# Performance work log

Measured on AMD Instinct MI355X. Metric: run time of the kernel, lower is better.

The kernel has to match this reference:

```python
import jax, jax.numpy as jnp
import numpy as np

N, E, T = 20000, 320000, 64
INP, EMB, OUT = 128, 16, 3
HEADS, MSIZE, MDIM, KDIM, VDIM = 4, 1024, 128, 64, 64


def setup_inputs() -> dict:
    key = jax.random.key(0)
    ks = iter(jax.random.split(key, 64))

    def nrm(shape, s=0.05):
        return jax.random.normal(next(ks), shape, dtype=jnp.float32) * s

    return dict(
        x=jax.random.normal(next(ks), (N, INP), dtype=jnp.float32),
        edge_index=jax.random.randint(next(ks), (2, E), 0, N),
        index=5,
        inp_types=jax.random.randint(next(ks), (T,), 0, 4),
        log_return=jax.random.normal(next(ks), (T,), dtype=jnp.float32),
        # SAGEConv 1 (SoftmaxAggregation temp t1, lin_l/lin_r, bias=False)
        t1=jnp.ones((1, INP), jnp.float32),
        W1l=nrm((INP, 512)), W1r=nrm((INP, 512)),
        ln1g_w=jnp.ones((512,), jnp.float32), ln1g_b=jnp.zeros((512,), jnp.float32),
        # SAGEConv 2
        t2=jnp.ones((1, 512), jnp.float32),
        W2l=nrm((512, 256)), W2r=nrm((512, 256)),
        ln2g_w=jnp.ones((256,), jnp.float32), ln2g_b=jnp.zeros((256,), jnp.float32),
        # MemPooling(256,128,heads=4,num_clusters=1)
        mp_k=nrm((HEADS, 1, 256), 1.0),
        mp_conv=nrm((HEADS,), 0.5),            # Conv2d(heads,1,1,bias=False)
        mp_lin=nrm((256, 128)),                # Linear(in,out,bias=False)
        fxg_w=nrm((128, 256)), fxg_b=jnp.zeros((256,), jnp.float32),
        # PolicyNet head
        emb=nrm((4, EMB), 1.0),
        fk_w=nrm((256, KDIM)), fk_b=jnp.zeros((KDIM,), jnp.float32),
        fv_w=nrm((256, VDIM)), fv_b=jnp.zeros((VDIM,), jnp.float32),
        # MultiHeadMemory
        mem=nrm((HEADS, MSIZE, MDIM), 1.0),
        mfk_w=nrm((MDIM, KDIM)), mfk_b=jnp.zeros((KDIM,), jnp.float32),
        mfv_w=nrm((MDIM, VDIM)), mfv_b=jnp.zeros((VDIM,), jnp.float32),
        mfx_w=nrm((VDIM * HEADS, VDIM)), mfx_b=jnp.zeros((VDIM,), jnp.float32),
        f1_w=nrm((INP + EMB + 2 * VDIM + 1, 512)),
        n1_w=jnp.ones((512,), jnp.float32), n1_b=jnp.zeros((512,), jnp.float32),
        f2_w=nrm((512, 256)),
        n2_w=jnp.ones((256,), jnp.float32), n2_b=jnp.zeros((256,), jnp.float32),
        f3_w=nrm((256, OUT)), f3_b=jnp.zeros((OUT,), jnp.float32),
    )


def _forward(x, t1, W1l, W1r, ln1g_w, ln1g_b, t2, W2l, W2r, ln2g_w, ln2g_b,
             mp_k, mp_conv, mp_lin, fxg_w, fxg_b, emb, fk_w, fk_b, fv_w, fv_b,
             mem, mfk_w, mfk_b, mfv_w, mfv_b, mfx_w, mfx_b,
             f1_w, n1_w, n1_b, f2_w, n2_w, n2_b, f3_w, f3_b,
             log_return, edge_index, inp_types, index):
    n = x.shape[0]
    src, dst = edge_index[0], edge_index[1]

    def sage(h, t, Wl, Wr):
        hj = h[src]                                    # [E, C] gather
        gate = hj * t                                  # learned softmax temperature
        m = jax.ops.segment_max(gate, dst, num_segments=n)
        e = jnp.exp(gate - m[dst])                     # segment-stable softmax
        s = jax.ops.segment_sum(e, dst, num_segments=n)
        agg = jax.ops.segment_sum(hj * (e / s[dst]), dst, num_segments=n)
        return agg @ Wl + h @ Wr                       # SAGEConv, bias=False

    def graph_ln(h, w, b, eps=1e-5):                   # PyG LayerNorm, mode='graph'
        hc = h - jnp.mean(h)
        return hc / jnp.sqrt(jnp.mean(hc * hc) + eps) * w + b

    h = jax.nn.relu(graph_ln(sage(x, t1, W1l, W1r), ln1g_w, ln1g_b))
    h = jax.nn.relu(graph_ln(sage(h, t2, W2l, W2r), ln2g_w, ln2g_b))

    # MemPooling (single graph => B=1), tau=1: student-t kernel over sq. distances
    H, K, C = mp_k.shape
    kk = mp_k.reshape(H * K, C)
    d2 = jnp.maximum(jnp.sum(kk * kk, 1)[:, None] - 2.0 * (kk @ h.T)
                     + jnp.sum(h * h, 1)[None, :], 0.0)        # [H*K, N]
    dist = 1.0 / (1.0 + d2)
    dist = dist.reshape(H, K, n).transpose(0, 2, 1)[None]      # [1, H, N, K]
    S = dist / jnp.sum(dist, -1, keepdims=True)
    S = jax.nn.softmax(jnp.einsum('h,bhnk->bnk', mp_conv, S), axis=-1)  # [1, N, K]
    zp = jnp.einsum('bnk,nc->bkc', S, h)[:, 0, :]              # squeeze(1), K==1
    z = (zp @ mp_lin) @ fxg_w + fxg_b                          # [1, 256]

    q = jax.nn.softmax(z @ fk_w + fk_b, axis=-1)               # [1, key_dim]
    v = z @ fv_w + fv_b                                        # [1, val_dim]

    # MultiHeadMemory
    km = jax.nn.softmax(mem @ mfk_w + mfk_b, axis=-1)          # [H, M, key]
    vm = mem @ mfv_w + mfv_b                                   # [H, M, val]
    w = jax.nn.softmax(jnp.einsum('bk,hnk->bhn', q, km), axis=-1)
    mv = jnp.einsum('bhn,hnv->bhv', w, vm).reshape(q.shape[0], -1)
    m_out = mv @ mfx_w + mfx_b                                 # [1, val]

    zz = jnp.concatenate([v, m_out], axis=-1)                  # [1, 2*val]
    t_len = inp_types.shape[0]
    xi = jnp.broadcast_to(x[index][None, :], (t_len, x.shape[1]))
    zb = jnp.broadcast_to(zz, (t_len, zz.shape[1]))
    feat = jnp.concatenate([xi, emb[inp_types], log_return.reshape(-1, 1), zb], axis=-1)

    def ln(h2, w2, b2, eps=1e-5):                              # nn.LayerNorm (last dim)
        mu = jnp.mean(h2, -1, keepdims=True)
        hc = h2 - mu
        return hc / jnp.sqrt(jnp.mean(hc * hc, -1, keepdims=True) + eps) * w2 + b2

    h1 = jax.nn.relu(ln(feat @ f1_w, n1_w, n1_b))              # dropout = identity (eval)
    h2 = jax.nn.relu(ln(h1 @ f2_w, n2_w, n2_b))
    return jax.nn.softmax(h2 @ f3_w + f3_b, axis=-1)           # [T, out_dim]


def reference(x, edge_index, index, inp_types, log_return, t1, W1l, W1r, ln1g_w, ln1g_b,
              t2, W2l, W2r, ln2g_w, ln2g_b, mp_k, mp_conv, mp_lin, fxg_w, fxg_b, emb,
              fk_w, fk_b, fv_w, fv_b, mem, mfk_w, mfk_b, mfv_w, mfv_b, mfx_w, mfx_b,
              f1_w, n1_w, n1_b, f2_w, n2_w, n2_b, f3_w, f3_b):
    return _forward(x, t1, W1l, W1r, ln1g_w, ln1g_b, t2, W2l, W2r, ln2g_w, ln2g_b,
                    mp_k, mp_conv, mp_lin, fxg_w, fxg_b, emb, fk_w, fk_b, fv_w, fv_b,
                    mem, mfk_w, mfk_b, mfv_w, mfv_b, mfx_w, mfx_b,
                    f1_w, n1_w, n1_b, f2_w, n2_w, n2_b, f3_w, f3_b,
                    log_return, edge_index, inp_types, index)
```

## Files before the change

kernel.cpp:

```cpp
#include <hip/hip_runtime.h>

typedef __attribute__((ext_vector_type(8))) short bf16x8;
typedef __attribute__((ext_vector_type(8))) unsigned short ushort8_t;
typedef __attribute__((ext_vector_type(4))) float f32x4;

__device__ __forceinline__ unsigned short f2bf(float f) {
    unsigned int x = __float_as_uint(f);
    unsigned int r = x + 0x7fffu + ((x >> 16) & 1u);
    return (unsigned short)(r >> 16);
}
__device__ __forceinline__ float bf2f(unsigned short u) {
    return __uint_as_float(((unsigned int)u) << 16);
}
__device__ __forceinline__ float fexp2(float x) { return __builtin_amdgcn_exp2f(x); }

#define LOG2E 1.44269504089f

__global__ __launch_bounds__(256) void prep_kernel(
    const int* __restrict__ dst, int E, int* __restrict__ counts,
    const float* __restrict__ x, unsigned short* __restrict__ xb, size_t nx4,
    const float* __restrict__ W1l, const float* __restrict__ W1r, unsigned short* __restrict__ Bt1,
    const float* __restrict__ W2l, const float* __restrict__ W2r, unsigned short* __restrict__ Bt2) {
    int i = blockIdx.x * 256 + threadIdx.x;
    int total = gridDim.x * 256;
    if (i < E) atomicAdd(&counts[dst[i]], 1);
    for (size_t j = i; j < nx4; j += total) {
        float4 v = *(const float4*)(x + j * 4);
        ushort4 o;
        o.x = f2bf(v.x); o.y = f2bf(v.y); o.z = f2bf(v.z); o.w = f2bf(v.w);
        *(ushort4*)(xb + j * 4) = o;
    }
    if (i < 512 * 256) {
        int nn = i >> 8, k = i & 255;
        float v = (k < 128) ? W1l[(size_t)k * 512 + nn] : W1r[(size_t)(k - 128) * 512 + nn];
        Bt1[i] = f2bf(v);
    }
    if (i < 256 * 1024) {
        int nn = i >> 10, k = i & 1023;
        float v = (k < 512) ? W2l[(size_t)k * 256 + nn] : W2r[(size_t)(k - 512) * 256 + nn];
        Bt2[i] = f2bf(v);
    }
}

template <int CHUNK>
__global__ __launch_bounds__(1024) void scan_kernel(int* __restrict__ cnt,
                                                    int* __restrict__ off, int n) {
    __shared__ int s[1024];
    int tid = threadIdx.x;
    int base = tid * CHUNK;
    int loc[CHUNK];
    int sum = 0;
#pragma unroll
    for (int i = 0; i < CHUNK; ++i) {
        int idx = base + i;
        int v = 0;
        if (idx < n) { v = cnt[idx]; cnt[idx] = 0; }
        sum += v;
        loc[i] = sum;
    }
    s[tid] = sum;
    __syncthreads();
    for (int d = 1; d < 1024; d <<= 1) {
        int t = (tid >= d) ? s[tid - d] : 0;
        __syncthreads();
        s[tid] += t;
        __syncthreads();
    }
    int prev = (tid > 0) ? s[tid - 1] : 0;
    if (tid == 0) off[0] = 0;
#pragma unroll
    for (int i = 0; i < CHUNK; ++i) {
        int idx = base + i;
        if (idx < n) off[idx + 1] = prev + loc[i];
    }
}

__global__ void fill_kernel(const int* __restrict__ src, const int* __restrict__ dst, int E,
                            const int* __restrict__ off, int* __restrict__ cursor,
                            int* __restrict__ srcs) {
    int i = blockIdx.x * 256 + threadIdx.x;
    if (i < E) {
        int d = dst[i];
        int p = atomicAdd(&cursor[d], 1);
        srcs[off[d] + p] = src[i];
    }
}

__global__ __launch_bounds__(256) void agg512s(const unsigned short* __restrict__ h,
                                               const float* __restrict__ t,
                                               const int* __restrict__ off,
                                               const int* __restrict__ srcs,
                                               unsigned short* __restrict__ agg, int n) {
    int wid = threadIdx.x >> 6, lane = threadIdx.x & 63;
    int node = blockIdx.x * 4 + wid;
    if (node >= n) return;
    int beg = off[node], end = off[node + 1];
    int col = blockIdx.y * 256 + lane * 4;
    float tc0 = t[col] * LOG2E, tc1 = t[col + 1] * LOG2E;
    float tc2 = t[col + 2] * LOG2E, tc3 = t[col + 3] * LOG2E;
    float sE0 = 0.f, sE1 = 0.f, sE2 = 0.f, sE3 = 0.f;
    float sW0 = 0.f, sW1 = 0.f, sW2 = 0.f, sW3 = 0.f;
#define P4(u)                                                        \
    {                                                                \
        float v0 = bf2f(u.x), v1 = bf2f(u.y);                        \
        float v2 = bf2f(u.z), v3 = bf2f(u.w);                        \
        float w0_ = fexp2(v0 * tc0), w1_ = fexp2(v1 * tc1);          \
        float w2_ = fexp2(v2 * tc2), w3_ = fexp2(v3 * tc3);          \
        sE0 += w0_; sW0 += v0 * w0_; sE1 += w1_; sW1 += v1 * w1_;    \
        sE2 += w2_; sW2 += v2 * w2_; sE3 += w3_; sW3 += v3 * w3_;    \
    }
    int e = beg;
    for (; e + 4 <= end; e += 4) {
        ushort4 u0 = *(const ushort4*)(h + (size_t)srcs[e] * 512 + col);
        ushort4 u1 = *(const ushort4*)(h + (size_t)srcs[e + 1] * 512 + col);
        ushort4 u2 = *(const ushort4*)(h + (size_t)srcs[e + 2] * 512 + col);
        ushort4 u3 = *(const ushort4*)(h + (size_t)srcs[e + 3] * 512 + col);
        P4(u0) P4(u1) P4(u2) P4(u3)
    }
    for (; e < end; ++e) {
        ushort4 u0 = *(const ushort4*)(h + (size_t)srcs[e] * 512 + col);
        P4(u0)
    }
#undef P4
    ushort4 o;
    o.x = f2bf((end > beg) ? (sW0 / sE0) : 0.f);
    o.y = f2bf((end > beg) ? (sW1 / sE1) : 0.f);
    o.z = f2bf((end > beg) ? (sW2 / sE2) : 0.f);
    o.w = f2bf((end > beg) ? (sW3 / sE3) : 0.f);
    *(ushort4*)(agg + (size_t)node * 512 + col) = o;
}

__global__ __launch_bounds__(256) void agg128(const unsigned short* __restrict__ h,
                                              const float* __restrict__ t,
                                              const int* __restrict__ off,
                                              const int* __restrict__ srcs,
                                              unsigned short* __restrict__ agg, int n) {
    int wid = threadIdx.x >> 6, lane = threadIdx.x & 63;
    int node = blockIdx.x * 4 + wid;
    if (node >= n) return;
    int beg = off[node], end = off[node + 1];
    int col = lane * 2;
    float t0 = t[col] * LOG2E, t1 = t[col + 1] * LOG2E;
    float e0 = 0.f, e1 = 0.f, w0 = 0.f, w1 = 0.f;
#define P2(u)                                          \
    {                                                  \
        float a = bf2f(u.x), b = bf2f(u.y);            \
        float xa = fexp2(a * t0), xb = fexp2(b * t1);  \
        e0 += xa; e1 += xb; w0 += a * xa; w1 += b * xb; \
    }
    int e = beg;
    for (; e + 4 <= end; e += 4) {
        ushort2 u0 = *(const ushort2*)(h + (size_t)srcs[e] * 128 + col);
        ushort2 u1 = *(const ushort2*)(h + (size_t)srcs[e + 1] * 128 + col);
        ushort2 u2 = *(const ushort2*)(h + (size_t)srcs[e + 2] * 128 + col);
        ushort2 u3 = *(const ushort2*)(h + (size_t)srcs[e + 3] * 128 + col);
        P2(u0) P2(u1) P2(u2) P2(u3)
    }
    for (; e < end; ++e) {
        ushort2 u0 = *(const ushort2*)(h + (size_t)srcs[e] * 128 + col);
        P2(u0)
    }
#undef P2
    ushort2 o;
    o.x = f2bf((end > beg) ? (w0 / e0) : 0.f);
    o.y = f2bf((end > beg) ? (w1 / e1) : 0.f);
    *(ushort2*)(agg + (size_t)node * 128 + col) = o;
}

__global__ __launch_bounds__(256) void gemm_dual_mfma3(
    const unsigned short* __restrict__ A1, const unsigned short* __restrict__ A2,
    const unsigned short* __restrict__ Bt,
    unsigned short* __restrict__ Cb, double* __restrict__ part,
    int M, int N, int K1, int K2) {
    const int Kc = K1 + K2;
    __shared__ unsigned short As[64 * 40];
    __shared__ unsigned short Bs[256 * 40];
    __shared__ double rs[256], rs2[256];
    int tid = threadIdx.x;
    int lane = tid & 63, w = tid >> 6;
    int m0 = blockIdx.y * 64, n0 = blockIdx.x * 256;
    f32x4 acc[4][4] = {};
    int kg = lane >> 4, lr = lane & 15;

    for (int k0 = 0; k0 < Kc; k0 += 32) {
        const unsigned short* Asrc;
        int kk, Ksrc;
        if (k0 < K1) { Asrc = A1; kk = k0; Ksrc = K1; }
        else         { Asrc = A2; kk = k0 - K1; Ksrc = K2; }
        {
            int r = tid >> 2, ch = tid & 3;
            int gr = m0 + r;
            ushort8_t v = {0, 0, 0, 0, 0, 0, 0, 0};
            if (gr < M) v = *(const ushort8_t*)(Asrc + (size_t)gr * Ksrc + kk + ch * 8);
            *(ushort8_t*)&As[r * 40 + ch * 8] = v;
        }
#pragma unroll
        for (int it = 0; it < 4; ++it) {
            int idx = tid + it * 256;
            int r = idx >> 2, ch = idx & 3;
            const unsigned short* srcp = Bt + (size_t)(n0 + r) * Kc + k0 + ch * 8;
            *(ushort8_t*)&Bs[r * 40 + ch * 8] = *(const ushort8_t*)srcp;
        }
        __syncthreads();
        bf16x8 a[4], b[4];
#pragma unroll
        for (int i = 0; i < 4; ++i)
            a[i] = *(bf16x8*)&As[(i * 16 + lr) * 40 + kg * 8];
#pragma unroll
        for (int j = 0; j < 4; ++j)
            b[j] = *(bf16x8*)&Bs[(w * 64 + j * 16 + lr) * 40 + kg * 8];
#pragma unroll
        for (int i = 0; i < 4; ++i)
#pragma unroll
            for (int j = 0; j < 4; ++j)
                acc[i][j] = __builtin_amdgcn_mfma_f32_16x16x32_bf16(a[i], b[j], acc[i][j], 0, 0, 0);
        __syncthreads();
    }
    double s = 0, s2 = 0;
#pragma unroll
    for (int i = 0; i < 4; ++i) {
        int rbase = m0 + i * 16 + kg * 4;
#pragma unroll
        for (int j = 0; j < 4; ++j) {
            int col = n0 + w * 64 + j * 16 + lr;
#pragma unroll
            for (int reg = 0; reg < 4; ++reg) {
                int row = rbase + reg;
                if (row < M) {
                    float v = acc[i][j][reg];
                    Cb[(size_t)row * N + col] = f2bf(v);
                    s += v;
                    s2 += (double)v * v;
                }
            }
        }
    }
    rs[tid] = s;
    rs2[tid] = s2;
    __syncthreads();
    for (int d = 128; d; d >>= 1) {
        if (tid < d) { rs[tid] += rs[tid + d]; rs2[tid] += rs2[tid + d]; }
        __syncthreads();
    }
    if (tid == 0) {
        int bid = blockIdx.y * gridDim.x + blockIdx.x;
        part[bid * 2] = rs[0];
        part[bid * 2 + 1] = rs2[0];
    }
}

template <int C>
__global__ __launch_bounds__(256) void ln_relu_ip(unsigned short* __restrict__ z,
                                                  const float* __restrict__ w,
                                                  const float* __restrict__ b,
                                                  const double* __restrict__ part, int nb,
                                                  float invn, size_t n) {
    __shared__ float st[2];
    if (threadIdx.x < 64) {
        double s = 0, s2 = 0;
        for (int i = threadIdx.x; i < nb; i += 64) { s += part[2 * i]; s2 += part[2 * i + 1]; }
        for (int d = 32; d; d >>= 1) { s += __shfl_down(s, d); s2 += __shfl_down(s2, d); }
        if (threadIdx.x == 0) {
            float mu = (float)(s * invn);
            float var = (float)(s2 * invn) - mu * mu;
            st[0] = mu;
            st[1] = rsqrtf(var + 1e-5f);
        }
    }
    __syncthreads();
    float mu = st[0], inv = st[1];
    size_t stride = (size_t)gridDim.x * 256 * 4;
    for (size_t i = ((size_t)blockIdx.x * 256 + threadIdx.x) * 4; i < n; i += stride) {
        ushort4 v = *(const ushort4*)(z + i);
        int c = (int)(i & (C - 1));
        ushort4 o;
        o.x = f2bf(fmaxf((bf2f(v.x) - mu) * inv * w[c] + b[c], 0.f));
        o.y = f2bf(fmaxf((bf2f(v.y) - mu) * inv * w[c + 1] + b[c + 1], 0.f));
        o.z = f2bf(fmaxf((bf2f(v.z) - mu) * inv * w[c + 2] + b[c + 2], 0.f));
        o.w = f2bf(fmaxf((bf2f(v.w) - mu) * inv * w[c + 3] + b[c + 3], 0.f));
        *(ushort4*)(z + i) = o;
    }
}

__global__ __launch_bounds__(256) void ln_colsum(const unsigned short* __restrict__ z2,
                                                 const float* __restrict__ w,
                                                 const float* __restrict__ b,
                                                 const double* __restrict__ part, int nb,
                                                 float invn, int n,
                                                 float* __restrict__ cspartT) {
    __shared__ float red[8 * 256];
    __shared__ float st[2];
    int tid = threadIdx.x;
    if (tid < 64) {
        double s = 0, s2 = 0;
        for (int i = tid; i < nb; i += 64) { s += part[2 * i]; s2 += part[2 * i + 1]; }
        for (int d = 32; d; d >>= 1) { s += __shfl_down(s, d); s2 += __shfl_down(s2, d); }
        if (tid == 0) {
            float mu = (float)(s * invn);
            float var = (float)(s2 * invn) - mu * mu;
            st[0] = mu;
            st[1] = rsqrtf(var + 1e-5f);
        }
    }
    __syncthreads();
    float mu = st[0], inv = st[1];
    int cg = tid & 31;
    int rl = tid >> 5;
    int c8 = cg * 8;
    float lw[8], lb[8];
#pragma unroll
    for (int i = 0; i < 8; ++i) { lw[i] = w[c8 + i] * inv; lb[i] = b[c8 + i] - mu * inv * w[c8 + i]; }
    int rows_per = (n + gridDim.x - 1) / gridDim.x;
    int r0 = blockIdx.x * rows_per;
    int r1 = min(n, r0 + rows_per);
    float acc[8] = {};
    for (int r = r0 + rl; r < r1; r += 8) {
        ushort8_t u = *(const ushort8_t*)(z2 + (size_t)r * 256 + c8);
#pragma unroll
        for (int i = 0; i < 8; ++i) acc[i] += fmaxf(bf2f(u[i]) * lw[i] + lb[i], 0.f);
    }
#pragma unroll
    for (int i = 0; i < 8; ++i) red[rl * 256 + c8 + i] = acc[i];
    __syncthreads();
    float s = 0;
#pragma unroll
    for (int r = 0; r < 8; ++r) s += red[r * 256 + tid];
    cspartT[tid * 64 + blockIdx.x] = s;
}

__global__ __launch_bounds__(256) void zqv_kernel(const float* __restrict__ cspartT,
                                                  const float* __restrict__ mp_lin,
                                                  const float* __restrict__ fxg_w,
                                                  const float* __restrict__ fxg_b,
                                                  const float* __restrict__ fk_w,
                                                  const float* __restrict__ fk_b,
                                                  const float* __restrict__ fv_w,
                                                  const float* __restrict__ fv_b,
                                                  float* __restrict__ qv) {
    __shared__ float zp_s[256], u_s[128], z_s[256], ql_s[64];
    __shared__ float part_s[1024];
    int tid = threadIdx.x;
    {
        float s = 0;
        const float* p = cspartT + tid * 64;
#pragma unroll
        for (int i = 0; i < 16; ++i) {
            float4 v = *(const float4*)(p + i * 4);
            s += v.x + v.y + v.z + v.w;
        }
        zp_s[tid] = s;
    }
    __syncthreads();
    {
        int og = tid & 31, kc = tid >> 5;
        int j4 = og * 4;
        f32x4 a = {0.f, 0.f, 0.f, 0.f};
        for (int ci = 0; ci < 32; ++ci) {
            int c = kc * 32 + ci;
            float4 w = *(const float4*)(mp_lin + (size_t)c * 128 + j4);
            float zc = zp_s[c];
            a[0] += zc * w.x; a[1] += zc * w.y; a[2] += zc * w.z; a[3] += zc * w.w;
        }
#pragma unroll
        for (int i = 0; i < 4; ++i) part_s[kc * 128 + j4 + i] = a[i];
    }
    __syncthreads();
    if (tid < 128) {
        float s = 0;
#pragma unroll
        for (int kc = 0; kc < 8; ++kc) s += part_s[kc * 128 + tid];
        u_s[tid] = s;
    }
    __syncthreads();
    {
        int og = tid & 63, kc = tid >> 6;
        int j4 = og * 4;
        f32x4 a = {0.f, 0.f, 0.f, 0.f};
        for (int ci = 0; ci < 32; ++ci) {
            int c = kc * 32 + ci;
            float4 w = *(const float4*)(fxg_w + (size_t)c * 256 + j4);
            float uc = u_s[c];
            a[0] += uc * w.x; a[1] += uc * w.y; a[2] += uc * w.z; a[3] += uc * w.w;
        }
#pragma unroll
        for (int i = 0; i < 4; ++i) part_s[kc * 256 + j4 + i] = a[i];
    }
    __syncthreads();
    {
        float s = fxg_b[tid];
#pragma unroll
        for (int kc = 0; kc < 4; ++kc) s += part_s[kc * 256 + tid];
        z_s[tid] = s;
    }
    __syncthreads();
    {
        int og = tid & 15, kc = tid >> 4;
        int j4 = og * 4;
        f32x4 a = {0.f, 0.f, 0.f, 0.f};
        for (int ci = 0; ci < 16; ++ci) {
            int c = kc * 16 + ci;
            float4 w = *(const float4*)(fk_w + (size_t)c * 64 + j4);
            float zc = z_s[c];
            a[0] += zc * w.x; a[1] += zc * w.y; a[2] += zc * w.z; a[3] += zc * w.w;
        }
#pragma unroll
        for (int i = 0; i < 4; ++i) part_s[kc * 64 + j4 + i] = a[i];
    }
    __syncthreads();
    if (tid < 64) {
        float s = fk_b[tid];
#pragma unroll
        for (int kc = 0; kc < 16; ++kc) s += part_s[kc * 64 + tid];
        ql_s[tid] = s;
    }
    __syncthreads();
    {
        int og = tid & 15, kc = tid >> 4;
        int j4 = og * 4;
        f32x4 a = {0.f, 0.f, 0.f, 0.f};
        for (int ci = 0; ci < 16; ++ci) {
            int c = kc * 16 + ci;
            float4 w = *(const float4*)(fv_w + (size_t)c * 64 + j4);
            float zc = z_s[c];
            a[0] += zc * w.x; a[1] += zc * w.y; a[2] += zc * w.z; a[3] += zc * w.w;
        }
#pragma unroll
        for (int i = 0; i < 4; ++i) part_s[kc * 64 + j4 + i] = a[i];
    }
    __syncthreads();
    if (tid < 64) {
        float mx = ql_s[tid];
        for (int d = 32; d; d >>= 1) mx = fmaxf(mx, __shfl_xor(mx, d));
        float e = __expf(ql_s[tid] - mx);
        float s = e;
        for (int d = 32; d; d >>= 1) s += __shfl_xor(s, d);
        qv[tid] = e / s;
        float vv = fv_b[tid];
#pragma unroll
        for (int kc = 0; kc < 16; ++kc) vv += part_s[kc * 64 + tid];
        qv[64 + tid] = vv;
    }
}

__global__ __launch_bounds__(256) void mem_kv_logit(const float* __restrict__ mem,
                                                    const float* __restrict__ mfk_w,
                                                    const float* __restrict__ mfk_b,
                                                    const float* __restrict__ mfv_w,
                                                    const float* __restrict__ mfv_b,
                                                    const float* __restrict__ qv,
                                                    float* __restrict__ logits,
                                                    float* __restrict__ vm) {
    __shared__ float rows[4][128];
    __shared__ float qs[64];
    int tid = threadIdx.x;
    int r0 = blockIdx.x * 4;
    if (tid < 64) qs[tid] = qv[tid];
    for (int i = tid; i < 512; i += 256) rows[i >> 7][i & 127] = mem[(size_t)r0 * 128 + i];
    __syncthreads();
    int lr = tid >> 6;
    int lane = tid & 63;
    const float* row = rows[lr];
    float kl = mfk_b[lane], vl = mfv_b[lane];
#pragma unroll 8
    for (int c = 0; c < 128; ++c) {
        float rv = row[c];
        kl += rv * mfk_w[c * 64 + lane];
        vl += rv * mfv_w[c * 64 + lane];
    }
    float mx = kl;
    for (int d = 32; d; d >>= 1) mx = fmaxf(mx, __shfl_xor(mx, d));
    float e = __expf(kl - mx);
    float s = e;
    for (int d = 32; d; d >>= 1) s += __shfl_xor(s, d);
    float kval = e / s;
    float wl = kval * qs[lane];
    for (int d = 32; d; d >>= 1) wl += __shfl_xor(wl, d);
    size_t gr = (size_t)(r0 + lr);
    if (lane == 0) logits[gr] = wl;
    vm[gr * 64 + lane] = vl;
}

__global__ __launch_bounds__(256) void attend_part(const float* __restrict__ logits,
                                                   const float* __restrict__ vm,
                                                   float* __restrict__ part) {
    int b = blockIdx.x;
    int h = b >> 4;
    int s0 = (b & 15) * 64;
    int tid = threadIdx.x;
    __shared__ float els[64];
    __shared__ float pr[4][64];
    __shared__ float lmax_s, lsum_s;
    if (tid < 64) {
        float lg = logits[h * 1024 + s0 + tid];
        float m = lg;
        for (int d = 32; d; d >>= 1) m = fmaxf(m, __shfl_xor(m, d));
        float e = __expf(lg - m);
        els[tid] = e;
        float s = e;
        for (int d = 32; d; d >>= 1) s += __shfl_xor(s, d);
        if (tid == 0) { lmax_s = m; lsum_s = s; }
    }
    __syncthreads();
    int dd = tid & 63, g = tid >> 6;
    float acc = 0;
    for (int s = g; s < 64; s += 4)
        acc += els[s] * vm[((size_t)h * 1024 + s0 + s) * 64 + dd];
    pr[g][dd] = acc;
    __syncthreads();
    if (tid < 64) {
        float pv = pr[0][tid] + pr[1][tid] + pr[2][tid] + pr[3][tid];
        part[b * 66 + 2 + tid] = pv;
        if (tid == 0) { part[b * 66] = lmax_s; part[b * 66 + 1] = lsum_s; }
    }
}

__device__ __forceinline__ float block_sum_256(float v, float* red) {
    int tid = threadIdx.x;
    red[tid] = v;
    __syncthreads();
    for (int d = 128; d; d >>= 1) { if (tid < d) red[tid] += red[tid + d]; __syncthreads(); }
    float r = red[0];
    __syncthreads();
    return r;
}

__global__ __launch_bounds__(256) void head_kernel(
    const float* __restrict__ x, const int* __restrict__ index_p,
    const int* __restrict__ inp_types, const float* __restrict__ log_return,
    const float* __restrict__ emb, const float* __restrict__ qv,
    const float* __restrict__ apart, const float* __restrict__ mfx_w,
    const float* __restrict__ mfx_b, const float* __restrict__ f1_w,
    const float* __restrict__ n1_w, const float* __restrict__ n1_b,
    const float* __restrict__ f2_w, const float* __restrict__ n2_w,
    const float* __restrict__ n2_b, const float* __restrict__ f3_w,
    const float* __restrict__ f3_b, float* __restrict__ out) {
    __shared__ float feat[273];
    __shared__ float h1[512];
    __shared__ float h2[256];
    __shared__ float red[256];
    __shared__ float l3[3];
    __shared__ float mv_s[256];
    __shared__ float mpart[1024];
    __shared__ float m_out_s[64];
    int r = blockIdx.x, tid = threadIdx.x;
    int idx = index_p[0];
    {
        int h = tid >> 6, dd = tid & 63;
        float gmax = -1e30f;
#pragma unroll
        for (int p = 0; p < 16; ++p) gmax = fmaxf(gmax, apart[(h * 16 + p) * 66]);
        float total = 0.f, acc = 0.f;
#pragma unroll
        for (int p = 0; p < 16; ++p) {
            float sc = __expf(apart[(h * 16 + p) * 66] - gmax);
            total += apart[(h * 16 + p) * 66 + 1] * sc;
            acc += apart[(h * 16 + p) * 66 + 2 + dd] * sc;
        }
        mv_s[h * 64 + dd] = acc / total;
    }
    __syncthreads();
    {
        int og = tid & 15, kc = tid >> 4;
        int j4 = og * 4;
        f32x4 a = {0.f, 0.f, 0.f, 0.f};
        for (int ci = 0; ci < 16; ++ci) {
            int c = kc * 16 + ci;
            float4 w = *(const float4*)(mfx_w + (size_t)c * 64 + j4);
            float mc = mv_s[c];
            a[0] += mc * w.x; a[1] += mc * w.y; a[2] += mc * w.z; a[3] += mc * w.w;
        }
#pragma unroll
        for (int i = 0; i < 4; ++i) mpart[kc * 64 + j4 + i] = a[i];
    }
    __syncthreads();
    if (tid < 64) {
        float s = mfx_b[tid];
#pragma unroll
        for (int kc = 0; kc < 16; ++kc) s += mpart[kc * 64 + tid];
        m_out_s[tid] = s;
    }
    __syncthreads();
    for (int i = tid; i < 273; i += 256) {
        float val;
        if (i < 128) val = x[(size_t)idx * 128 + i];
        else if (i < 144) val = emb[inp_types[r] * 16 + (i - 128)];
        else if (i == 144) val = log_return[r];
        else if (i < 209) val = qv[64 + (i - 145)];
        else val = m_out_s[i - 209];
        feat[i] = val;
    }
    __syncthreads();
    float a0 = 0, a1 = 0;
    for (int c = 0; c < 273; ++c) {
        float f = feat[c];
        a0 += f * f1_w[c * 512 + tid];
        a1 += f * f1_w[c * 512 + tid + 256];
    }
    float mu = block_sum_256(a0 + a1, red) / 512.f;
    float c0 = a0 - mu, c1 = a1 - mu;
    float var = block_sum_256(c0 * c0 + c1 * c1, red) / 512.f;
    float inv = rsqrtf(var + 1e-5f);
    h1[tid] = fmaxf(c0 * inv * n1_w[tid] + n1_b[tid], 0.f);
    h1[tid + 256] = fmaxf(c1 * inv * n1_w[tid + 256] + n1_b[tid + 256], 0.f);
    __syncthreads();
    float b0 = 0;
    for (int c = 0; c < 512; ++c) b0 += h1[c] * f2_w[c * 256 + tid];
    float mu2 = block_sum_256(b0, red) / 256.f;
    float cc = b0 - mu2;
    float var2 = block_sum_256(cc * cc, red) / 256.f;
    float inv2 = rsqrtf(var2 + 1e-5f);
    h2[tid] = fmaxf(cc * inv2 * n2_w[tid] + n2_b[tid], 0.f);
    __syncthreads();
    if (tid < 3) {
        float a = f3_b[tid];
        for (int c = 0; c < 256; ++c) a += h2[c] * f3_w[c * 3 + tid];
        l3[tid] = a;
    }
    __syncthreads();
    if (tid < 3) {
        float mx = fmaxf(l3[0], fmaxf(l3[1], l3[2]));
        float s = __expf(l3[0] - mx) + __expf(l3[1] - mx) + __expf(l3[2] - mx);
        out[r * 3 + tid] = __expf(l3[tid] - mx) / s;
    }
}

extern "C" void kernel_launch(void* const* d_in, const int* in_sizes, int n_in,
                              void* d_out, int out_size, void* d_ws, size_t ws_size,
                              hipStream_t stream) {
    const float* x = (const float*)d_in[0];
    const int* ei = (const int*)d_in[1];
    const int* index_p = (const int*)d_in[2];
    const int* inp_types = (const int*)d_in[3];
    const float* log_return = (const float*)d_in[4];
    const float* t1 = (const float*)d_in[5];
    const float* W1l = (const float*)d_in[6];
    const float* W1r = (const float*)d_in[7];
    const float* ln1g_w = (const float*)d_in[8];
    const float* ln1g_b = (const float*)d_in[9];
    const float* t2 = (const float*)d_in[10];
    const float* W2l = (const float*)d_in[11];
    const float* W2r = (const float*)d_in[12];
    const float* ln2g_w = (const float*)d_in[13];
    const float* ln2g_b = (const float*)d_in[14];
    const float* mp_lin = (const float*)d_in[17];
    const float* fxg_w = (const float*)d_in[18];
    const float* fxg_b = (const float*)d_in[19];
    const float* emb = (const float*)d_in[20];
    const float* fk_w = (const float*)d_in[21];
    const float* fk_b = (const float*)d_in[22];
    const float* fv_w = (const float*)d_in[23];
    const float* fv_b = (const float*)d_in[24];
    const float* mem = (const float*)d_in[25];
    const float* mfk_w = (const float*)d_in[26];
    const float* mfk_b = (const float*)d_in[27];
    const float* mfv_w = (const float*)d_in[28];
    const float* mfv_b = (const float*)d_in[29];
    const float* mfx_w = (const float*)d_in[30];
    const float* mfx_b = (const float*)d_in[31];
    const float* f1_w = (const float*)d_in[32];
    const float* n1_w = (const float*)d_in[33];
    const float* n1_b = (const float*)d_in[34];
    const float* f2_w = (const float*)d_in[35];
    const float* n2_w = (const float*)d_in[36];
    const float* n2_b = (const float*)d_in[37];
    const float* f3_w = (const float*)d_in[38];
    const float* f3_b = (const float*)d_in[39];
    float* out = (float*)d_out;

    int n = in_sizes[0] / 128;
    int E = in_sizes[1] / 2;
    int T = in_sizes[3];
    const int* src = ei;
    const int* dst = ei + E;

    char* w = (char*)d_ws;
    auto alloc = [&](size_t bytes) {
        char* p = w;
        w += (bytes + 255) & ~(size_t)255;
        return p;
    };
    int* counts = (int*)alloc((size_t)n * 4);
    int* off = (int*)alloc((size_t)(n + 1) * 4);
    int* srcs = (int*)alloc((size_t)E * 4);
    unsigned short* xb = (unsigned short*)alloc((size_t)n * 128 * 2);
    unsigned short* agg1b = (unsigned short*)alloc((size_t)n * 128 * 2);
    unsigned short* z1b = (unsigned short*)alloc((size_t)n * 512 * 2);
    unsigned short* agg2b = (unsigned short*)alloc((size_t)n * 512 * 2);
    unsigned short* z2b = (unsigned short*)alloc((size_t)n * 256 * 2);
    double* partd = (double*)alloc(2048 * 2 * 8);
    float* cspartT = (float*)alloc(256 * 64 * 4);
    float* qv = (float*)alloc(128 * 4);
    float* logits = (float*)alloc((size_t)4 * 1024 * 4);
    float* vm = (float*)alloc((size_t)4 * 1024 * 64 * 4);
    float* apart = (float*)alloc(64 * 66 * 4);
    unsigned short* Bt1 = (unsigned short*)alloc((size_t)512 * 256 * 2);
    unsigned short* Bt2 = (unsigned short*)alloc((size_t)256 * 1024 * 2);

    int nblk_e = (E + 255) / 256;
    int mblk64 = (n + 63) / 64;

    hipMemsetAsync(counts, 0, (size_t)n * 4, stream);
    prep_kernel<<<nblk_e, 256, 0, stream>>>(dst, E, counts, x, xb, (size_t)n * 128 / 4,
                                            W1l, W1r, Bt1, W2l, W2r, Bt2);
    scan_kernel<20><<<1, 1024, 0, stream>>>(counts, off, n);
    fill_kernel<<<nblk_e, 256, 0, stream>>>(src, dst, E, off, counts, srcs);

    agg128<<<(n + 3) / 4, 256, 0, stream>>>(xb, t1, off, srcs, agg1b, n);
    gemm_dual_mfma3<<<dim3(2, mblk64), 256, 0, stream>>>(agg1b, xb, Bt1, z1b, partd, n, 512, 128, 128);
    ln_relu_ip<512><<<1024, 256, 0, stream>>>(z1b, ln1g_w, ln1g_b, partd, 2 * mblk64,
                                              1.0f / ((float)n * 512.f), (size_t)n * 512);

    agg512s<<<dim3((n + 3) / 4, 2), 256, 0, stream>>>(z1b, t2, off, srcs, agg2b, n);
    gemm_dual_mfma3<<<dim3(1, mblk64), 256, 0, stream>>>(agg2b, z1b, Bt2, z2b, partd, n, 256, 512, 512);

    ln_colsum<<<64, 256, 0, stream>>>(z2b, ln2g_w, ln2g_b, partd, mblk64,
                                      1.0f / ((float)n * 256.f), n, cspartT);
    zqv_kernel<<<1, 256, 0, stream>>>(cspartT, mp_lin, fxg_w, fxg_b, fk_w, fk_b, fv_w, fv_b, qv);

    mem_kv_logit<<<1024, 256, 0, stream>>>(mem, mfk_w, mfk_b, mfv_w, mfv_b, qv, logits, vm);
    attend_part<<<64, 256, 0, stream>>>(logits, vm, apart);

    head_kernel<<<T, 256, 0, stream>>>(x, index_p, inp_types, log_return, emb, qv, apart,
                                       mfx_w, mfx_b, f1_w, n1_w, n1_b, f2_w, n2_w, n2_b,
                                       f3_w, f3_b, out);
}
```

Baseline: 287.2 us.

## Factor shared f1 projection out of per-row head kernel into pre-kernel

The head's first linear layer is split algebraically. The row-invariant part (x[index], qv, memory output) is computed once in a new 2-block pre-kernel, along with per-type embedding projections for the 4 types. Each of the 64 row blocks then only adds base, the type projection and log_return times one weight row, instead of redoing a 273x512 matvec. The f2 matvec is also reworked to use float4 loads with a 4-way K split reduced through shared memory. This adds one kernel launch and a small global round trip.

```diff
diff --git a/kernel.cpp b/kernel.cpp
--- a/kernel.cpp
+++ b/kernel.cpp
@@ -514,35 +514,16 @@
     }
 }
 
-__device__ __forceinline__ float block_sum_256(float v, float* red) {
-    int tid = threadIdx.x;
-    red[tid] = v;
-    __syncthreads();
-    for (int d = 128; d; d >>= 1) { if (tid < d) red[tid] += red[tid + d]; __syncthreads(); }
-    float r = red[0];
-    __syncthreads();
-    return r;
-}
-
-__global__ __launch_bounds__(256) void head_kernel(
+__global__ __launch_bounds__(256) void head_pre(
     const float* __restrict__ x, const int* __restrict__ index_p,
-    const int* __restrict__ inp_types, const float* __restrict__ log_return,
-    const float* __restrict__ emb, const float* __restrict__ qv,
-    const float* __restrict__ apart, const float* __restrict__ mfx_w,
-    const float* __restrict__ mfx_b, const float* __restrict__ f1_w,
-    const float* __restrict__ n1_w, const float* __restrict__ n1_b,
-    const float* __restrict__ f2_w, const float* __restrict__ n2_w,
-    const float* __restrict__ n2_b, const float* __restrict__ f3_w,
-    const float* __restrict__ f3_b, float* __restrict__ out) {
-    __shared__ float feat[273];
-    __shared__ float h1[512];
-    __shared__ float h2[256];
-    __shared__ float red[256];
-    __shared__ float l3[3];
+    const float* __restrict__ qv, const float* __restrict__ apart,
+    const float* __restrict__ mfx_w, const float* __restrict__ mfx_b,
+    const float* __restrict__ emb, const float* __restrict__ f1_w,
+    float* __restrict__ base, float* __restrict__ tp) {
     __shared__ float mv_s[256];
     __shared__ float mpart[1024];
-    __shared__ float m_out_s[64];
-    int r = blockIdx.x, tid = threadIdx.x;
+    __shared__ float fsh[256];
+    int tid = threadIdx.x;
     int idx = index_p[0];
     {
         int h = tid >> 6, dd = tid & 63;
@@ -573,38 +554,103 @@
         for (int i = 0; i < 4; ++i) mpart[kc * 64 + j4 + i] = a[i];
     }
     __syncthreads();
-    if (tid < 64) {
-        float s = mfx_b[tid];
-#pragma unroll
-        for (int kc = 0; kc < 16; ++kc) s += mpart[kc * 64 + tid];
-        m_out_s[tid] = s;
-    }
-    __syncthreads();
-    for (int i = tid; i < 273; i += 256) {
-        float val;
-        if (i < 128) val = x[(size_t)idx * 128 + i];
-        else if (i < 144) val = emb[inp_types[r] * 16 + (i - 128)];
-        else if (i == 144) val = log_return[r];
-        else if (i < 209) val = qv[64 + (i - 145)];
-        else val = m_out_s[i - 209];
-        feat[i] = val;
-    }
-    __syncthreads();
-    float a0 = 0, a1 = 0;
-    for (int c = 0; c < 273; ++c) {
-        float f = feat[c];
-        a0 += f * f1_w[c * 512 + tid];
-        a1 += f * f1_w[c * 512 + tid + 256];
-    }
-    float mu = block_sum_256(a0 + a1, red) / 512.f;
-    float c0 = a0 - mu, c1 = a1 - mu;
+    if (tid < 128) fsh[tid] = x[(size_t)idx * 128 + tid];
+    else if (tid < 192) fsh[tid] = qv[64 + (tid - 128)];
+    else {
+        int dd = tid - 192;
+        float s = mfx_b[dd];
+#pragma unroll
+        for (int kc = 0; kc < 16; ++kc) s += mpart[kc * 64 + dd];
+        fsh[tid] = s;
+    }
+    __syncthreads();
+    int j = blockIdx.x * 256 + tid;
+    float a0 = 0, a1 = 0, a2 = 0, a3 = 0;
+#pragma unroll 4
+    for (int c = 0; c < 128; c += 4) {
+        a0 += fsh[c] * f1_w[(size_t)c * 512 + j];
+        a1 += fsh[c + 1] * f1_w[(size_t)(c + 1) * 512 + j];
+        a2 += fsh[c + 2] * f1_w[(size_t)(c + 2) * 512 + j];
+        a3 += fsh[c + 3] * f1_w[(size_t)(c + 3) * 512 + j];
+    }
+#pragma unroll 4
+    for (int i = 0; i < 64; i += 4) {
+        a0 += fsh[128 + i] * f1_w[(size_t)(145 + i) * 512 + j];
+        a1 += fsh[129 + i] * f1_w[(size_t)(146 + i) * 512 + j];
+        a2 += fsh[130 + i] * f1_w[(size_t)(147 + i) * 512 + j];
+        a3 += fsh[131 + i] * f1_w[(size_t)(148 + i) * 512 + j];
+    }
+#pragma unroll 4
+    for (int i = 0; i < 64; i += 4) {
+        a0 += fsh[192 + i] * f1_w[(size_t)(209 + i) * 512 + j];
+        a1 += fsh[193 + i] * f1_w[(size_t)(210 + i) * 512 + j];
+        a2 += fsh[194 + i] * f1_w[(size_t)(211 + i) * 512 + j];
+        a3 += fsh[195 + i] * f1_w[(size_t)(212 + i) * 512 + j];
+    }
+    base[j] = (a0 + a1) + (a2 + a3);
+#pragma unroll
+    for (int t = 0; t < 4; ++t) {
+        float s0 = 0, s1 = 0;
+#pragma unroll
+        for (int k = 0; k < 16; k += 2) {
+            s0 += emb[t * 16 + k] * f1_w[(size_t)(128 + k) * 512 + j];
+            s1 += emb[t * 16 + k + 1] * f1_w[(size_t)(129 + k) * 512 + j];
+        }
+        tp[t * 512 + j] = s0 + s1;
+    }
+}
+
+__device__ __forceinline__ float block_sum_256(float v, float* red) {
+    int tid = threadIdx.x;
+    red[tid] = v;
+    __syncthreads();
+    for (int d = 128; d; d >>= 1) { if (tid < d) red[tid] += red[tid + d]; __syncthreads(); }
+    float r = red[0];
+    __syncthreads();
+    return r;
+}
+
+__global__ __launch_bounds__(256) void head_main(
+    const int* __restrict__ inp_types, const float* __restrict__ log_return,
+    const float* __restrict__ base, const float* __restrict__ tp,
+    const float* __restrict__ f1_w, const float* __restrict__ n1_w,
+    const float* __restrict__ n1_b, const float* __restrict__ f2_w,
+    const float* __restrict__ n2_w, const float* __restrict__ n2_b,
+    const float* __restrict__ f3_w, const float* __restrict__ f3_b,
+    float* __restrict__ out) {
+    __shared__ float h1[512];
+    __shared__ float h2[256];
+    __shared__ float red[256];
+    __shared__ float part_s[1024];
+    __shared__ float l3[3];
+    int r = blockIdx.x, tid = threadIdx.x;
+    int ty = inp_types[r];
+    float lr = log_return[r];
+    float p0 = base[tid] + tp[ty * 512 + tid] + lr * f1_w[(size_t)144 * 512 + tid];
+    float p1 = base[tid + 256] + tp[ty * 512 + tid + 256] + lr * f1_w[(size_t)144 * 512 + tid + 256];
+    float mu = block_sum_256(p0 + p1, red) / 512.f;
+    float c0 = p0 - mu, c1 = p1 - mu;
     float var = block_sum_256(c0 * c0 + c1 * c1, red) / 512.f;
     float inv = rsqrtf(var + 1e-5f);
     h1[tid] = fmaxf(c0 * inv * n1_w[tid] + n1_b[tid], 0.f);
     h1[tid + 256] = fmaxf(c1 * inv * n1_w[tid + 256] + n1_b[tid + 256], 0.f);
     __syncthreads();
-    float b0 = 0;
-    for (int c = 0; c < 512; ++c) b0 += h1[c] * f2_w[c * 256 + tid];
+    {
+        int og = tid & 63, kc = tid >> 6;
+        int j4 = og * 4;
+        f32x4 a = {0.f, 0.f, 0.f, 0.f};
+#pragma unroll 2
+        for (int ci = 0; ci < 128; ++ci) {
+            int c = kc * 128 + ci;
+            float4 w = *(const float4*)(f2_w + (size_t)c * 256 + j4);
+            float hc = h1[c];
+            a[0] += hc * w.x; a[1] += hc * w.y; a[2] += hc * w.z; a[3] += hc * w.w;
+        }
+#pragma unroll
+        for (int i = 0; i < 4; ++i) part_s[kc * 256 + j4 + i] = a[i];
+    }
+    __syncthreads();
+    float b0 = part_s[tid] + part_s[256 + tid] + part_s[512 + tid] + part_s[768 + tid];
     float mu2 = block_sum_256(b0, red) / 256.f;
     float cc = b0 - mu2;
     float var2 = block_sum_256(cc * cc, red) / 256.f;
@@ -693,6 +739,8 @@
     float* logits = (float*)alloc((size_t)4 * 1024 * 4);
     float* vm = (float*)alloc((size_t)4 * 1024 * 64 * 4);
     float* apart = (float*)alloc(64 * 66 * 4);
+    float* hbase = (float*)alloc(512 * 4);
+    float* htp = (float*)alloc(4 * 512 * 4);
     unsigned short* Bt1 = (unsigned short*)alloc((size_t)512 * 256 * 2);
     unsigned short* Bt2 = (unsigned short*)alloc((size_t)256 * 1024 * 2);
 
@@ -720,7 +768,7 @@
     mem_kv_logit<<<1024, 256, 0, stream>>>(mem, mfk_w, mfk_b, mfv_w, mfv_b, qv, logits, vm);
     attend_part<<<64, 256, 0, stream>>>(logits, vm, apart);
 
-    head_kernel<<<T, 256, 0, stream>>>(x, index_p, inp_types, log_return, emb, qv, apart,
-                                       mfx_w, mfx_b, f1_w, n1_w, n1_b, f2_w, n2_w, n2_b,
-                                       f3_w, f3_b, out);
-}
+    head_pre<<<2, 256, 0, stream>>>(x, index_p, qv, apart, mfx_w, mfx_b, emb, f1_w, hbase, htp);
+    head_main<<<T, 256, 0, stream>>>(inp_types, log_return, hbase, htp, f1_w, n1_w, n1_b,
+                                     f2_w, n2_w, n2_b, f3_w, f3_b, out);
+}
```

New measurement: 290.6 us. No clear change (+1.2%).
